# Optimization experiments

Hardware: AMD Instinct MI355X
Metric: run time of the kernel (lower is better)

Reference implementation:

```python
import jax, jax.numpy as jnp
import numpy as np

D_MODEL = 1024
HIDDEN = 64
N_STEPS = 6
T0, T1 = 0.0, 1.0


def setup_inputs() -> dict:
    key = jax.random.key(0)
    kx, k1, k2, k3, k4 = jax.random.split(key, 5)
    # PyTorch nn.Linear default init: U(-1/sqrt(fan_in), 1/sqrt(fan_in))
    s1 = 1.0 / np.sqrt(D_MODEL + 1)
    s2 = 1.0 / np.sqrt(HIDDEN)
    return {
        "x": jax.random.normal(kx, (8, 2048, D_MODEL), dtype=jnp.float32),
        "W1": jax.random.uniform(k1, (D_MODEL + 1, HIDDEN), jnp.float32, -s1, s1),
        "b1": jax.random.uniform(k2, (HIDDEN,), jnp.float32, -s1, s1),
        "W2": jax.random.uniform(k3, (HIDDEN, D_MODEL), jnp.float32, -s2, s2),
        "b2": jax.random.uniform(k4, (D_MODEL,), jnp.float32, -s2, s2),
    }


def _dynamics(t, z, W1, b1, W2, b2):
    # Equivalent to concat([z, t*ones], -1) @ W1: split the last row of W1
    # (the time channel) so we avoid materializing the concat.
    h = jnp.tanh(jnp.einsum("btd,dh->bth", z, W1[:-1]) + t * W1[-1] + b1)
    return jnp.einsum("bth,hd->btd", h, W2) + b2


def reference(x, W1, b1, W2, b2):
    h = (T1 - T0) / N_STEPS  # step size
    ts = T0 + h * jnp.arange(N_STEPS, dtype=x.dtype)

    def rk4_step(z, t):
        k1 = _dynamics(t, z, W1, b1, W2, b2)
        k2 = _dynamics(t + h / 2, z + (h / 2) * k1, W1, b1, W2, b2)
        k3 = _dynamics(t + h / 2, z + (h / 2) * k2, W1, b1, W2, b2)
        k4 = _dynamics(t + h, z + h * k3, W1, b1, W2, b2)
        z_next = z + (h / 6) * (k1 + 2 * k2 + 2 * k3 + k4)
        return z_next, None

    z_T, _ = jax.lax.scan(rk4_step, x, ts)
    return z_T
```

## Files before the change

### kernel.cpp

```cpp
#include <hip/hip_runtime.h>
#include <hip/hip_bf16.h>

#define DM 1024
#define HID 64
#define NSTEP 6
#define RSTEP (1.0f/6.0f)

using short8  = __attribute__((ext_vector_type(8))) short;
using short4v = __attribute__((ext_vector_type(4))) short;
using f32x4   = __attribute__((ext_vector_type(4))) float;

#define WS_W1P 0
#define WS_W2P 131072
#define WS_GP  262144
#define WS_U   270336
#define WS_VST 270592
#define WS_HU  276736

#define L_H   0
#define L_VST 2304
#define L_HU  8448
#define LDS_TOTAL 8704
#define HP 144

#define FENCE() asm volatile("s_waitcnt lgkmcnt(0)" ::: "memory")

__device__ __forceinline__ short f2bf(float f) {
    __hip_bfloat16 h = __float2bfloat16(f);
    short s;
    __builtin_memcpy(&s, &h, 2);
    return s;
}
__device__ __forceinline__ float ftanh(float x) {
    x = fminf(fmaxf(x, -10.f), 10.f);
    float e = __expf(2.f * x);
    return __fdividef(e - 1.f, e + 1.f);
}

__global__ void k_prep(const float* __restrict__ W1, const float* __restrict__ W2,
                       const float* __restrict__ b1, const float* __restrict__ b2,
                       short* __restrict__ W1P, short* __restrict__ W2P,
                       short* __restrict__ GP, float* __restrict__ U,
                       float* __restrict__ VST, float* __restrict__ HU) {
    __shared__ float red[4][64];
    int b = blockIdx.x;
    int t = threadIdx.x;
    int l = t & 63, q4 = t >> 6;
    if (b < 128) {
        if (t < 64) {
            int kk = b >> 2, c = b & 3;
            int col = c * 16 + (l & 15);
            int kb = kk * 32 + ((l >> 4) << 3);
            short8 v;
            #pragma unroll
            for (int i = 0; i < 8; ++i) v[i] = f2bf(W1[(kb + i) * HID + col]);
            *(short8*)(W1P + (((kk * 4 + c) * 64) + l) * 8) = v;
        }
    } else if (b < 256) {
        if (t < 64) {
            int bb = b - 128;
            int kk2 = bb >> 6, ct = bb & 63;
            int col = ct * 16 + (l & 15);
            int kb = kk2 * 32 + ((l >> 4) << 3);
            short8 v;
            #pragma unroll
            for (int i = 0; i < 8; ++i) v[i] = f2bf(W2[(kb + i) * DM + col]);
            *(short8*)(W2P + (((kk2 * 64 + ct) * 64) + l) * 8) = v;
        }
    } else if (b < 320) {
        int j = b - 256;
        float acc = 0.f;
        #pragma unroll 8
        for (int d = q4 * 256; d < q4 * 256 + 256; ++d)
            acc += W2[j * DM + d] * W1[d * HID + l];
        red[q4][l] = acc;
        __syncthreads();
        if (t < 64) {
            float a = red[0][l] + red[1][l] + red[2][l] + red[3][l];
            int kk = j >> 5, lk = (j >> 3) & 3, ii = j & 7, c = l >> 4, lo = l & 15;
            GP[(((kk * 4 + c) * 64) + lk * 16 + lo) * 8 + ii] = f2bf(a);
        }
    } else {
        float acc = 0.f;
        #pragma unroll 8
        for (int d = q4 * 256; d < q4 * 256 + 256; ++d)
            acc += b2[d] * W1[d * HID + l];
        red[q4][l] = acc;
        __syncthreads();
        if (t < 64) {
            float uu = red[0][l] + red[1][l] + red[2][l] + red[3][l];
            U[l] = uu;
            HU[l] = RSTEP * uu;
            float b1l = b1[l];
            float wtl = W1[DM * HID + l];
            #pragma unroll
            for (int s6 = 0; s6 < 6; ++s6) {
                float ts = RSTEP * (float)s6;
                float tm = ts + 0.5f * RSTEP;
                float vmid = b1l + tm * wtl + 0.5f * RSTEP * uu;
                VST[(s6 * 4 + 0) * 64 + l] = b1l + ts * wtl;
                VST[(s6 * 4 + 1) * 64 + l] = vmid;
                VST[(s6 * 4 + 2) * 64 + l] = vmid;
                VST[(s6 * 4 + 3) * 64 + l] = b1l + (ts + RSTEP) * wtl + RSTEP * uu;
            }
        }
    }
}

__global__ __launch_bounds__(64) __attribute__((amdgpu_waves_per_eu(2, 4)))
void k_ode(
        const float* __restrict__ X, const float* __restrict__ b2,
        const short* __restrict__ W1P, const short* __restrict__ W2P,
        const short* __restrict__ GP, const float* __restrict__ VST,
        const float* __restrict__ HU, float* __restrict__ OUT) {
    extern __shared__ char smem[];
    const int lane = threadIdx.x & 63;
    const int hq = lane >> 4;
    const int l15 = lane & 15;
    const size_t row0 = (size_t)blockIdx.x * 16;
    const float* xrow = X + (row0 + l15) * DM;

    #pragma unroll
    for (int i = 0; i < 6; ++i)
        *(f32x4*)(smem + L_VST + i * 1024 + lane * 16) =
            *(const f32x4*)(VST + i * 256 + lane * 4);
    if (lane < 16)
        *(f32x4*)(smem + L_HU + lane * 16) = *(const f32x4*)(HU + lane * 4);

    short8 gfr[2][4];
    #pragma unroll
    for (int k2 = 0; k2 < 2; ++k2)
        #pragma unroll
        for (int c = 0; c < 4; ++c)
            gfr[k2][c] = *(const short8*)(GP + ((k2 * 4 + c) * 64 + lane) * 8);

    f32x4 sz[4] = {(f32x4){0.f,0.f,0.f,0.f}, (f32x4){0.f,0.f,0.f,0.f},
                   (f32x4){0.f,0.f,0.f,0.f}, (f32x4){0.f,0.f,0.f,0.f}};
    {
        const short8* wp = (const short8*)W1P;
        #pragma unroll 4
        for (int kk = 0; kk < 32; ++kk) {
            const float* xp = xrow + (kk << 5) + (hq << 3);
            f32x4 lo = *(const f32x4*)(xp);
            f32x4 hi = *(const f32x4*)(xp + 4);
            short8 zf;
            #pragma unroll
            for (int j = 0; j < 4; ++j) { zf[j] = f2bf(lo[j]); zf[4 + j] = f2bf(hi[j]); }
            #pragma unroll
            for (int c = 0; c < 4; ++c)
                sz[c] = __builtin_amdgcn_mfma_f32_16x16x32_bf16(
                            wp[(kk * 4 + c) * 64 + lane], zf, sz[c], 0, 0, 0);
        }
    }

    f32x4 ssum[4] = {(f32x4){0.f,0.f,0.f,0.f}, (f32x4){0.f,0.f,0.f,0.f},
                     (f32x4){0.f,0.f,0.f,0.f}, (f32x4){0.f,0.f,0.f,0.f}};

    for (int s = 0; s < NSTEP; ++s) {
        f32x4 hsum[4];

        #pragma unroll
        for (int c = 0; c < 4; ++c) {
            f32x4 vst = *(const f32x4*)(smem + L_VST + (s * 4 + 0) * 256 + c * 64 + (hq << 4));
            short4v hc;
            #pragma unroll
            for (int j = 0; j < 4; ++j) {
                float h = ftanh(sz[c][j] + vst[j]);
                hsum[c][j] = h;
                hc[j] = f2bf(h);
            }
            *(short4v*)(smem + L_H + l15 * HP + c * 32 + (hq << 3)) = hc;
        }
        FENCE();

        #pragma unroll
        for (int e = 1; e < 4; ++e) {
            const float ce = (e == 3) ? RSTEP : (0.5f * RSTEP);
            const float we = (e == 3) ? 1.f : 2.f;
            short8 hf0 = *(const short8*)(smem + L_H + l15 * HP + (hq << 4));
            short8 hf1 = *(const short8*)(smem + L_H + l15 * HP + 64 + (hq << 4));
            #pragma unroll
            for (int c = 0; c < 4; ++c) {
                f32x4 dd = (f32x4){0.f, 0.f, 0.f, 0.f};
                dd = __builtin_amdgcn_mfma_f32_16x16x32_bf16(gfr[0][c], hf0, dd, 0, 0, 0);
                dd = __builtin_amdgcn_mfma_f32_16x16x32_bf16(gfr[1][c], hf1, dd, 0, 0, 0);
                f32x4 vst = *(const f32x4*)(smem + L_VST + (s * 4 + e) * 256 + c * 64 + (hq << 4));
                short4v hc;
                #pragma unroll
                for (int j = 0; j < 4; ++j) {
                    float h = ftanh(sz[c][j] + ce * dd[j] + vst[j]);
                    hsum[c][j] += we * h;
                    if (e < 3) {
                        hc[j] = f2bf(h);
                    } else {
                        ssum[c][j] += hsum[c][j] * (RSTEP / 6.f);
                        hc[j] = (s < NSTEP - 1) ? f2bf(hsum[c][j] * (RSTEP / 6.f))
                                                : f2bf(ssum[c][j]);
                    }
                }
                *(short4v*)(smem + L_H + l15 * HP + c * 32 + (hq << 3)) = hc;
            }
            FENCE();
        }

        if (s < NSTEP - 1) {
            short8 hb0 = *(const short8*)(smem + L_H + l15 * HP + (hq << 4));
            short8 hb1 = *(const short8*)(smem + L_H + l15 * HP + 64 + (hq << 4));
            #pragma unroll
            for (int c = 0; c < 4; ++c) {
                f32x4 d = (f32x4){0.f, 0.f, 0.f, 0.f};
                d = __builtin_amdgcn_mfma_f32_16x16x32_bf16(gfr[0][c], hb0, d, 0, 0, 0);
                d = __builtin_amdgcn_mfma_f32_16x16x32_bf16(gfr[1][c], hb1, d, 0, 0, 0);
                f32x4 hu4 = *(const f32x4*)(smem + L_HU + c * 64 + (hq << 4));
                #pragma unroll
                for (int j = 0; j < 4; ++j)
                    sz[c][j] += d[j] + hu4[j];
            }
        }
    }

    {
        short8 sb0 = *(const short8*)(smem + L_H + l15 * HP + (hq << 4));
        short8 sb1 = *(const short8*)(smem + L_H + l15 * HP + 64 + (hq << 4));
        const short8* w2p8 = (const short8*)W2P;
        float* orow = OUT + (row0 + l15) * DM;
        #pragma unroll 4
        for (int ct = 0; ct < 64; ++ct) {
            short8 wa = w2p8[ct * 64 + lane];
            short8 wb = w2p8[(64 + ct) * 64 + lane];
            f32x4 p = (f32x4){0.f, 0.f, 0.f, 0.f};
            p = __builtin_amdgcn_mfma_f32_16x16x32_bf16(wa, sb0, p, 0, 0, 0);
            p = __builtin_amdgcn_mfma_f32_16x16x32_bf16(wb, sb1, p, 0, 0, 0);
            int col = ct * 16 + (hq << 2);
            f32x4 xv  = *(const f32x4*)(xrow + col);
            f32x4 b2v = *(const f32x4*)(b2 + col);
            f32x4 nv;
            #pragma unroll
            for (int j = 0; j < 4; ++j)
                nv[j] = xv[j] + p[j] + b2v[j];
            *(f32x4*)(orow + col) = nv;
        }
    }
}

extern "C" void kernel_launch(void* const* d_in, const int* in_sizes, int n_in,
                              void* d_out, int out_size, void* d_ws, size_t ws_size,
                              hipStream_t stream) {
    (void)in_sizes; (void)n_in; (void)out_size; (void)ws_size;
    const float* X  = (const float*)d_in[0];
    const float* W1 = (const float*)d_in[1];
    const float* b1 = (const float*)d_in[2];
    const float* W2 = (const float*)d_in[3];
    const float* b2 = (const float*)d_in[4];
    float* OUT = (float*)d_out;
    short* W1P = (short*)((char*)d_ws + WS_W1P);
    short* W2P = (short*)((char*)d_ws + WS_W2P);
    short* GP  = (short*)((char*)d_ws + WS_GP);
    float* U   = (float*)((char*)d_ws + WS_U);
    float* VST = (float*)((char*)d_ws + WS_VST);
    float* HU  = (float*)((char*)d_ws + WS_HU);

    k_prep<<<321, 256, 0, stream>>>(W1, W2, b1, b2, W1P, W2P, GP, U, VST, HU);
    k_ode<<<1024, 64, LDS_TOTAL, stream>>>(X, b2, W1P, W2P, GP, VST, HU, OUT);
}
```

Measured before the change: 84.27 us.

## Software-pipeline epilogue loads, batch x prologue loads, stage b2 in LDS, compact prep grid

New measurement: 72.14 us. 14.4% less time.

```diff
diff --git a/kernel.cpp b/kernel.cpp
--- a/kernel.cpp
+++ b/kernel.cpp
@@ -20,7 +20,8 @@
 #define L_H   0
 #define L_VST 2304
 #define L_HU  8448
-#define LDS_TOTAL 8704
+#define L_B2  8704
+#define LDS_TOTAL 12800
 #define HP 144
 
 #define FENCE() asm volatile("s_waitcnt lgkmcnt(0)" ::: "memory")
@@ -46,29 +47,25 @@
     int b = blockIdx.x;
     int t = threadIdx.x;
     int l = t & 63, q4 = t >> 6;
-    if (b < 128) {
-        if (t < 64) {
-            int kk = b >> 2, c = b & 3;
-            int col = c * 16 + (l & 15);
-            int kb = kk * 32 + ((l >> 4) << 3);
-            short8 v;
-            #pragma unroll
-            for (int i = 0; i < 8; ++i) v[i] = f2bf(W1[(kb + i) * HID + col]);
-            *(short8*)(W1P + (((kk * 4 + c) * 64) + l) * 8) = v;
-        }
-    } else if (b < 256) {
-        if (t < 64) {
-            int bb = b - 128;
-            int kk2 = bb >> 6, ct = bb & 63;
-            int col = ct * 16 + (l & 15);
-            int kb = kk2 * 32 + ((l >> 4) << 3);
-            short8 v;
-            #pragma unroll
-            for (int i = 0; i < 8; ++i) v[i] = f2bf(W2[(kb + i) * DM + col]);
-            *(short8*)(W2P + (((kk2 * 64 + ct) * 64) + l) * 8) = v;
-        }
-    } else if (b < 320) {
-        int j = b - 256;
+    if (b < 32) {
+        int kk = b, c = q4;
+        int col = c * 16 + (l & 15);
+        int kb = kk * 32 + ((l >> 4) << 3);
+        short8 v;
+        #pragma unroll
+        for (int i = 0; i < 8; ++i) v[i] = f2bf(W1[(kb + i) * HID + col]);
+        *(short8*)(W1P + (((kk * 4 + c) * 64) + l) * 8) = v;
+    } else if (b < 64) {
+        int unit = (b - 32) * 4 + q4;
+        int kk2 = unit >> 6, ct = unit & 63;
+        int col = ct * 16 + (l & 15);
+        int kb = kk2 * 32 + ((l >> 4) << 3);
+        short8 v;
+        #pragma unroll
+        for (int i = 0; i < 8; ++i) v[i] = f2bf(W2[(kb + i) * DM + col]);
+        *(short8*)(W2P + (((kk2 * 64 + ct) * 64) + l) * 8) = v;
+    } else if (b < 128) {
+        int j = b - 64;
         float acc = 0.f;
         #pragma unroll 8
         for (int d = q4 * 256; d < q4 * 256 + 256; ++d)
@@ -107,6 +104,26 @@
     }
 }
 
+#define EPL(W0,W1,W2,W3,X0,X1,P) \
+    W0 = w2p8[(P) * 64 + lane];        W1 = w2p8[((P) + 64) * 64 + lane]; \
+    W2 = w2p8[((P) + 1) * 64 + lane];  W3 = w2p8[((P) + 65) * 64 + lane]; \
+    X0 = *(const f32x4*)(xrow + (P) * 16 + (hq << 2)); \
+    X1 = *(const f32x4*)(xrow + ((P) + 1) * 16 + (hq << 2));
+
+#define EPC(W0,W1,W2,W3,X0,X1,P) { \
+    f32x4 p0 = (f32x4){0.f,0.f,0.f,0.f}, p1 = (f32x4){0.f,0.f,0.f,0.f}; \
+    p0 = __builtin_amdgcn_mfma_f32_16x16x32_bf16(W0, sb0, p0, 0, 0, 0); \
+    p0 = __builtin_amdgcn_mfma_f32_16x16x32_bf16(W1, sb1, p0, 0, 0, 0); \
+    p1 = __builtin_amdgcn_mfma_f32_16x16x32_bf16(W2, sb0, p1, 0, 0, 0); \
+    p1 = __builtin_amdgcn_mfma_f32_16x16x32_bf16(W3, sb1, p1, 0, 0, 0); \
+    f32x4 b0v = *(const f32x4*)(smem + L_B2 + ((P) * 16 + (hq << 2)) * 4); \
+    f32x4 b1v = *(const f32x4*)(smem + L_B2 + (((P) + 1) * 16 + (hq << 2)) * 4); \
+    f32x4 n0, n1; \
+    for (int j = 0; j < 4; ++j) { n0[j] = X0[j] + p0[j] + b0v[j]; \
+                                  n1[j] = X1[j] + p1[j] + b1v[j]; } \
+    *(f32x4*)(orow + (P) * 16 + (hq << 2)) = n0; \
+    *(f32x4*)(orow + ((P) + 1) * 16 + (hq << 2)) = n1; }
+
 __global__ __launch_bounds__(64) __attribute__((amdgpu_waves_per_eu(2, 4)))
 void k_ode(
         const float* __restrict__ X, const float* __restrict__ b2,
@@ -121,37 +138,50 @@
     const float* xrow = X + (row0 + l15) * DM;
 
     #pragma unroll
+    for (int i = 0; i < 4; ++i)
+        *(f32x4*)(smem + L_B2 + lane * 64 + i * 16) =
+            *(const f32x4*)(b2 + lane * 16 + i * 4);
+
+    f32x4 sz[4] = {(f32x4){0.f,0.f,0.f,0.f}, (f32x4){0.f,0.f,0.f,0.f},
+                   (f32x4){0.f,0.f,0.f,0.f}, (f32x4){0.f,0.f,0.f,0.f}};
+    {
+        const short8* wp = (const short8*)W1P;
+        #pragma unroll
+        for (int B = 0; B < 4; ++B) {
+            f32x4 lo[8], hi[8];
+            #pragma unroll
+            for (int i = 0; i < 8; ++i) {
+                const float* xp = xrow + ((B * 8 + i) << 5) + (hq << 3);
+                lo[i] = *(const f32x4*)(xp);
+                hi[i] = *(const f32x4*)(xp + 4);
+            }
+            #pragma unroll
+            for (int i = 0; i < 8; ++i) {
+                int kk = B * 8 + i;
+                short8 zf;
+                #pragma unroll
+                for (int j = 0; j < 4; ++j) { zf[j] = f2bf(lo[i][j]); zf[4 + j] = f2bf(hi[i][j]); }
+                #pragma unroll
+                for (int c = 0; c < 4; ++c)
+                    sz[c] = __builtin_amdgcn_mfma_f32_16x16x32_bf16(
+                                wp[(kk * 4 + c) * 64 + lane], zf, sz[c], 0, 0, 0);
+            }
+        }
+    }
+
+    #pragma unroll
     for (int i = 0; i < 6; ++i)
         *(f32x4*)(smem + L_VST + i * 1024 + lane * 16) =
             *(const f32x4*)(VST + i * 256 + lane * 4);
     if (lane < 16)
         *(f32x4*)(smem + L_HU + lane * 16) = *(const f32x4*)(HU + lane * 4);
-
     short8 gfr[2][4];
     #pragma unroll
     for (int k2 = 0; k2 < 2; ++k2)
         #pragma unroll
         for (int c = 0; c < 4; ++c)
             gfr[k2][c] = *(const short8*)(GP + ((k2 * 4 + c) * 64 + lane) * 8);
-
-    f32x4 sz[4] = {(f32x4){0.f,0.f,0.f,0.f}, (f32x4){0.f,0.f,0.f,0.f},
-                   (f32x4){0.f,0.f,0.f,0.f}, (f32x4){0.f,0.f,0.f,0.f}};
-    {
-        const short8* wp = (const short8*)W1P;
-        #pragma unroll 4
-        for (int kk = 0; kk < 32; ++kk) {
-            const float* xp = xrow + (kk << 5) + (hq << 3);
-            f32x4 lo = *(const f32x4*)(xp);
-            f32x4 hi = *(const f32x4*)(xp + 4);
-            short8 zf;
-            #pragma unroll
-            for (int j = 0; j < 4; ++j) { zf[j] = f2bf(lo[j]); zf[4 + j] = f2bf(hi[j]); }
-            #pragma unroll
-            for (int c = 0; c < 4; ++c)
-                sz[c] = __builtin_amdgcn_mfma_f32_16x16x32_bf16(
-                            wp[(kk * 4 + c) * 64 + lane], zf, sz[c], 0, 0, 0);
-        }
-    }
+    FENCE();
 
     f32x4 ssum[4] = {(f32x4){0.f,0.f,0.f,0.f}, (f32x4){0.f,0.f,0.f,0.f},
                      (f32x4){0.f,0.f,0.f,0.f}, (f32x4){0.f,0.f,0.f,0.f}};
@@ -224,21 +254,16 @@
         short8 sb1 = *(const short8*)(smem + L_H + l15 * HP + 64 + (hq << 4));
         const short8* w2p8 = (const short8*)W2P;
         float* orow = OUT + (row0 + l15) * DM;
-        #pragma unroll 4
-        for (int ct = 0; ct < 64; ++ct) {
-            short8 wa = w2p8[ct * 64 + lane];
-            short8 wb = w2p8[(64 + ct) * 64 + lane];
-            f32x4 p = (f32x4){0.f, 0.f, 0.f, 0.f};
-            p = __builtin_amdgcn_mfma_f32_16x16x32_bf16(wa, sb0, p, 0, 0, 0);
-            p = __builtin_amdgcn_mfma_f32_16x16x32_bf16(wb, sb1, p, 0, 0, 0);
-            int col = ct * 16 + (hq << 2);
-            f32x4 xv  = *(const f32x4*)(xrow + col);
-            f32x4 b2v = *(const f32x4*)(b2 + col);
-            f32x4 nv;
-            #pragma unroll
-            for (int j = 0; j < 4; ++j)
-                nv[j] = xv[j] + p[j] + b2v[j];
-            *(f32x4*)(orow + col) = nv;
+
+        short8 wA0, wA1, wA2, wA3; f32x4 xA0, xA1;
+        short8 wB0, wB1, wB2, wB3; f32x4 xB0, xB1;
+        EPL(wA0, wA1, wA2, wA3, xA0, xA1, 0)
+        #pragma unroll
+        for (int p = 0; p < 64; p += 4) {
+            EPL(wB0, wB1, wB2, wB3, xB0, xB1, p + 2)
+            EPC(wA0, wA1, wA2, wA3, xA0, xA1, p)
+            if (p + 4 < 64) { EPL(wA0, wA1, wA2, wA3, xA0, xA1, p + 4) }
+            EPC(wB0, wB1, wB2, wB3, xB0, xB1, p + 2)
         }
     }
 }
@@ -260,6 +285,6 @@
     float* VST = (float*)((char*)d_ws + WS_VST);
     float* HU  = (float*)((char*)d_ws + WS_HU);
 
-    k_prep<<<321, 256, 0, stream>>>(W1, W2, b1, b2, W1P, W2P, GP, U, VST, HU);
+    k_prep<<<129, 256, 0, stream>>>(W1, W2, b1, b2, W1P, W2P, GP, U, VST, HU);
     k_ode<<<1024, 64, LDS_TOTAL, stream>>>(X, b2, W1P, W2P, GP, VST, HU, OUT);
 }
```
